# Kernel tuning notes

Hardware: AMD Instinct MI355X
Metric: run time of the kernel (lower is better)

## Reference

```python
import jax, jax.numpy as jnp
import numpy as np

B_SZ, T, D_IN, D_STATE, D_OUT = 32, 4096, 128, 128, 128


def setup_inputs() -> dict:
    key = jax.random.key(0)
    k1, k2, k3, k4, k5 = jax.random.split(key, 5)
    inputs = jax.random.normal(k1, (B_SZ, T, D_IN), dtype=jnp.float32)
    # A ~ orthogonal initializer scaled to spectral radius 0.9 for a stable recurrence
    Araw = jax.random.normal(k2, (D_STATE, D_STATE), dtype=jnp.float32)
    Q, _ = jnp.linalg.qr(Araw)
    A = 0.9 * Q
    B = jax.random.normal(k3, (D_STATE, D_IN), dtype=jnp.float32) / np.sqrt(D_IN)
    C = jax.random.normal(k4, (D_OUT, D_STATE), dtype=jnp.float32) / np.sqrt(D_STATE)
    D = jax.random.normal(k5, (D_OUT, D_IN), dtype=jnp.float32) / np.sqrt(D_IN)
    return {"inputs": inputs, "A": A, "B": B, "C": C, "D": D}


def reference(inputs, A, B, C, D):
    """x(t+1) = A x(t) + B u(t);  y(t+1) = C x(t+1) + D u(t).
    x0 = 0, return_sequences=True -> output [batch, time, d_out]."""
    x0 = jnp.zeros((inputs.shape[0], A.shape[0]), dtype=inputs.dtype)
    u_tb = jnp.swapaxes(inputs, 0, 1)  # [T, batch, d_in]

    def step(x, u):
        x1 = x @ A.T + u @ B.T          # [batch, d_state]
        y1 = x1 @ C.T + u @ D.T         # [batch, d_out]
        return x1, y1

    _, ys = jax.lax.scan(step, x0, u_tb)
    return jnp.swapaxes(ys, 0, 1)       # [batch, T, d_out]
```

## Files before the change

### kernel.cpp

```cpp
#include <hip/hip_runtime.h>
#include <cstddef>
#include <cstdint>

#define DIM 128
#define T_LEN 4096
#define BATCH 32
#define L_CH 32
#define N_CH 128
#define N_CHAINS 4096
#define KFULL 4096

typedef float f32x4 __attribute__((ext_vector_type(4)));
typedef short s16x8 __attribute__((ext_vector_type(8)));
typedef unsigned short u16x4 __attribute__((ext_vector_type(4)));
typedef unsigned short u16x8 __attribute__((ext_vector_type(8)));
typedef unsigned int u32;

#define OFF_UBF  0
#define OFF_A64  8388608
#define OFF_A96  8404992
#define OFF_A128 8421376
#define OFF_VBF  8437760
#define OFF_MCBF 8716288
#define OFF_VP2  8757248
#define OFF_SBF  12582912
#define OFF_KBF  12845056
#define OFF_CABF 13107200
#define OFF_WBF  13377536
#define OFF_AP   13639680
#define OFF_CA   14180352
#define OFF_K    14704640
#define OFF_W    15228928
#define OFF_B    15753216
#define OFF_C    15769600
#define OFF_D    15785984
#define AP(d)    (OFF_AP + (d) * 16384)

__device__ __forceinline__ f32x4 ld_pin(const float* p) {
    return *reinterpret_cast<const volatile f32x4*>(p);
}
__device__ __forceinline__ unsigned short f2bf(float x) {
    u32 u = __builtin_bit_cast(u32, x);
    return (unsigned short)((u + 0x7FFFu + ((u >> 16) & 1u)) >> 16);
}
__device__ __forceinline__ void gld16(const void* g, void* l) {
    __builtin_amdgcn_global_load_lds((const __attribute__((address_space(1))) u32*)g,
                                     (__attribute__((address_space(3))) u32*)l, 16, 0, 0);
}

__global__ void k_init(const float* __restrict__ u, const float* __restrict__ A,
                       const float* __restrict__ B, const float* __restrict__ C,
                       const float* __restrict__ D, float* __restrict__ wsf) {
    if (blockIdx.x < 8192) {
        unsigned short* ubf = (unsigned short*)(wsf + OFF_UBF);
        const size_t e0 = (size_t)(blockIdx.x * 256 + threadIdx.x) * 8;
        const f32x4 v0 = *reinterpret_cast<const f32x4*>(u + e0);
        const f32x4 v1 = *reinterpret_cast<const f32x4*>(u + e0 + 4);
        u16x8 o;
        o[0] = f2bf(v0.x); o[1] = f2bf(v0.y); o[2] = f2bf(v0.z); o[3] = f2bf(v0.w);
        o[4] = f2bf(v1.x); o[5] = f2bf(v1.y); o[6] = f2bf(v1.z); o[7] = f2bf(v1.w);
        *reinterpret_cast<u16x8*>(ubf + e0) = o;
    } else {
        const int e0 = ((blockIdx.x - 8192) * 256 + threadIdx.x) * 4;
        const int mat = e0 >> 14, rem = e0 & 16383;
        const float* src = (mat == 0) ? A : (mat == 1) ? B : (mat == 2) ? C : D;
        const int dst = (mat == 0) ? AP(1) : (mat == 1) ? OFF_B : (mat == 2) ? OFF_C : OFF_D;
        *reinterpret_cast<f32x4*>(wsf + dst + rem) =
            *reinterpret_cast<const f32x4*>(src + rem);
    }
}

__global__ void k_castm2(float* __restrict__ wsf) {
    const int e0 = (blockIdx.x * 256 + threadIdx.x) * 4;
    unsigned short* MCBF = (unsigned short*)(wsf + OFF_MCBF);
    unsigned short* WBF  = (unsigned short*)(wsf + OFF_WBF);
    u16x4 o;
    unsigned short* dst;
    if (e0 < 81920) {
        const int irow = e0 / 640;
        const int rem  = e0 - irow * 640;
        const int e    = rem >> 7;
        const int k    = rem & 127;
        if (e == 0) {
#pragma unroll
            for (int j = 0; j < 4; ++j)
                o[j] = (k + j == irow) ? (unsigned short)0x3F80 : (unsigned short)0;
        } else {
            const int moff = (e == 1) ? AP(32) : (e == 2) ? OFF_A64
                           : (e == 3) ? OFF_A96 : OFF_A128;
            const f32x4 v = *reinterpret_cast<const f32x4*>(wsf + moff + irow * 128 + k);
            o[0] = f2bf(v.x); o[1] = f2bf(v.y); o[2] = f2bf(v.z); o[3] = f2bf(v.w);
        }
        dst = MCBF + e0;
    } else {
        const int widx = e0 - 81920;
        const int i = widx >> 7, k = widx & 127;
        const f32x4 v = *reinterpret_cast<const f32x4*>(wsf + OFF_B + i * 128 + k);
        o[0] = f2bf(v.x); o[1] = f2bf(v.y); o[2] = f2bf(v.z); o[3] = f2bf(v.w);
        dst = WBF + i * 4096 + 3968 + k;
    }
    *reinterpret_cast<u16x4*>(dst) = o;
}

struct MMDesc { int n; int xo[64]; int yo[64]; int oo[64]; int ao[64]; int bo[64]; int bs[64]; };

__global__ __launch_bounds__(256, 1) void k_mmb(float* __restrict__ wsf, MMDesc d) {
    const int mm = blockIdx.x >> 2, sub = blockIdx.x & 3;
    const float* X = wsf + d.xo[mm];
    const float* Y = wsf + d.yo[mm];
    float* O = wsf + d.oo[mm];
    const int ao = d.ao[mm];
    __shared__ __align__(16) float Ys[DIM][DIM];
    const int t = threadIdx.x;
#pragma unroll
    for (int i = 0; i < 16; ++i) {
        const int j = t + i * 256;
        reinterpret_cast<f32x4*>(&Ys[0][0])[j] = reinterpret_cast<const f32x4*>(Y)[j];
    }
    const int r = sub * 32 + (t >> 3);
    const int c0 = (t & 7) * 16;
    f32x4 xr[32];
#pragma unroll
    for (int k = 0; k < 32; ++k) xr[k] = ld_pin(&X[r * DIM + 4 * k]);
    __syncthreads();
    float acc[16];
#pragma unroll
    for (int j = 0; j < 16; ++j) acc[j] = 0.f;
#pragma unroll
    for (int k = 0; k < DIM; ++k) {
        const float xv = ((const float*)xr)[k];
#pragma unroll
        for (int j = 0; j < 16; j += 4) {
            const f32x4 yv = *reinterpret_cast<const f32x4*>(&Ys[k][c0 + j]);
            acc[j + 0] = fmaf(xv, yv.x, acc[j + 0]);
            acc[j + 1] = fmaf(xv, yv.y, acc[j + 1]);
            acc[j + 2] = fmaf(xv, yv.z, acc[j + 2]);
            acc[j + 3] = fmaf(xv, yv.w, acc[j + 3]);
        }
    }
    if (ao >= 0) {
        const float* Ad = wsf + ao;
#pragma unroll
        for (int j = 0; j < 16; ++j) acc[j] += Ad[r * DIM + c0 + j];
    }
#pragma unroll
    for (int j = 0; j < 16; j += 4) {
        f32x4 o; o.x = acc[j]; o.y = acc[j + 1]; o.z = acc[j + 2]; o.w = acc[j + 3];
        *reinterpret_cast<f32x4*>(&O[r * DIM + c0 + j]) = o;
    }
    if (d.bo[mm] >= 0) {
        unsigned short* bw = (unsigned short*)wsf + (size_t)d.bo[mm] + (size_t)r * d.bs[mm] + c0;
#pragma unroll
        for (int j = 0; j < 16; j += 4) {
            u16x4 ob;
            ob[0] = f2bf(acc[j]); ob[1] = f2bf(acc[j + 1]);
            ob[2] = f2bf(acc[j + 2]); ob[3] = f2bf(acc[j + 3]);
            *reinterpret_cast<u16x4*>(bw + j) = ob;
        }
    }
}

__global__ __launch_bounds__(256, 2) void k_gemm1(const unsigned short* __restrict__ UBF,
                                                  const unsigned short* __restrict__ WBF,
                                                  float* __restrict__ VP) {
    __shared__ __align__(16) unsigned short lsA[2][4096];
    __shared__ __align__(16) unsigned short lsB[2][4096];
    const int b = blockIdx.x >> 2, ksp = blockIdx.x & 3;
    const int t = threadIdx.x, w = t >> 6, l = t & 63;
    const int wr = w >> 1, wc = w & 1;
    const int m0 = b * 128;
    const int rowA0 = w * 32 + (l >> 2);
    const int scol8 = ((l & 3) ^ ((l >> 3) & 3)) * 8;
    const int rsw   = ((l >> 4) ^ ((l >> 1) & 3)) * 8;
    const int wvb = w * 1024;
    const int kb = ksp * 1024;

    f32x4 acc[4][4];
#pragma unroll
    for (int a = 0; a < 4; ++a)
#pragma unroll
        for (int c = 0; c < 4; ++c) acc[a][c] = (f32x4)(0.f);

#define STAGE1(q, buf) do {                                                        \
    const int kq = kb + (q) * 32 + scol8;                                          \
    const unsigned short* ga = UBF + (size_t)(m0 + rowA0) * KFULL + kq;            \
    const unsigned short* gb = WBF + (size_t)rowA0 * KFULL + kq;                   \
    gld16(ga, &lsA[buf][wvb]);  gld16(ga + 16 * KFULL, &lsA[buf][wvb + 512]);      \
    gld16(gb, &lsB[buf][wvb]);  gld16(gb + 16 * KFULL, &lsB[buf][wvb + 512]);      \
} while (0)

    STAGE1(0, 0);
    __syncthreads();
#pragma unroll 1
    for (int q = 0; q < 32; ++q) {
        const int buf = q & 1;
        if (q + 1 < 32) STAGE1(q + 1, buf ^ 1);
        s16x8 af[4], bfr[4];
#pragma unroll
        for (int mi = 0; mi < 4; ++mi)
            af[mi] = *(const s16x8*)(&lsA[buf][(wr * 64 + mi * 16 + (l & 15)) * 32 + rsw]);
#pragma unroll
        for (int ni = 0; ni < 4; ++ni)
            bfr[ni] = *(const s16x8*)(&lsB[buf][(wc * 64 + ni * 16 + (l & 15)) * 32 + rsw]);
#pragma unroll
        for (int mi = 0; mi < 4; ++mi)
#pragma unroll
            for (int ni = 0; ni < 4; ++ni)
                acc[mi][ni] = __builtin_amdgcn_mfma_f32_16x16x32_bf16(af[mi], bfr[ni], acc[mi][ni], 0, 0, 0);
        __syncthreads();
    }
    float* vp = VP + (size_t)ksp * (N_CHAINS * DIM);
    const int row0 = wr * 64 + (l >> 4) * 4;
    const int col0 = wc * 64 + (l & 15);
#pragma unroll
    for (int mi = 0; mi < 4; ++mi)
#pragma unroll
        for (int ni = 0; ni < 4; ++ni)
#pragma unroll
            for (int jj = 0; jj < 4; ++jj)
                vp[(size_t)(m0 + row0 + mi * 16 + jj) * DIM + col0 + ni * 16] = acc[mi][ni][jj];
#undef STAGE1
}

__global__ void k_vred(const float* __restrict__ VP, unsigned short* __restrict__ VBF) {
    if (blockIdx.x < 512) {
        const int g = (blockIdx.x * 256 + threadIdx.x) * 4;
        f32x4 s = *reinterpret_cast<const f32x4*>(VP + g);
#pragma unroll
        for (int sp = 1; sp < 4; ++sp) {
            const f32x4 v = *reinterpret_cast<const f32x4*>(VP + sp * 524288 + g);
            s.x += v.x; s.y += v.y; s.z += v.z; s.w += v.w;
        }
        const int m = g >> 7, i = g & 127;
        const int b = m >> 7, c = m & 127;
        u16x4 o;
        o[0] = f2bf(s.x); o[1] = f2bf(s.y); o[2] = f2bf(s.z); o[3] = f2bf(s.w);
        *reinterpret_cast<u16x4*>(VBF + b * 17408 + (8 + c) * 128 + i) = o;
    } else {
        const int z = ((blockIdx.x - 512) * 256 + threadIdx.x) * 4;
        const int b = z >> 10, rem = z & 1023;
        u16x4 zz; zz[0] = 0; zz[1] = 0; zz[2] = 0; zz[3] = 0;
        *reinterpret_cast<u16x4*>(VBF + b * 17408 + rem) = zz;
    }
}

__global__ __launch_bounds__(256, 2) void k_comb2(const unsigned short* __restrict__ VBF,
                                                  const unsigned short* __restrict__ MCBF,
                                                  unsigned short* __restrict__ SBF) {
    __shared__ __align__(16) unsigned short lsA[2][4096];
    __shared__ __align__(16) unsigned short lsB[2][4096];
    const int b = blockIdx.x;
    const int t = threadIdx.x, w = t >> 6, l = t & 63;
    const int wr = w >> 1, wc = w & 1;
    const int rowA0 = w * 32 + (l >> 2);
    const int scol8 = ((l & 3) ^ ((l >> 3) & 3)) * 8;
    const int rsw   = ((l >> 4) ^ ((l >> 1) & 3)) * 8;
    const int wvb = w * 1024;
    const unsigned short* Vb = VBF + b * 17408;

    f32x4 acc[4][4];
#pragma unroll
    for (int a = 0; a < 4; ++a)
#pragma unroll
        for (int c = 0; c < 4; ++c) acc[a][c] = (f32x4)(0.f);

#define STAGEC(q, buf) do {                                                        \
    const int kq = (q) * 32 + scol8;                                               \
    const int e = kq >> 7, kk = kq & 127;                                          \
    const unsigned short* ga = Vb + (8 + rowA0 - 1 - e) * 128 + kk;                \
    const unsigned short* gb = MCBF + rowA0 * 640 + kq;                            \
    gld16(ga, &lsA[buf][wvb]);  gld16(ga + 16 * 128, &lsA[buf][wvb + 512]);        \
    gld16(gb, &lsB[buf][wvb]);  gld16(gb + 16 * 640, &lsB[buf][wvb + 512]);        \
} while (0)

    STAGEC(0, 0);
    __syncthreads();
#pragma unroll 1
    for (int q = 0; q < 20; ++q) {
        const int buf = q & 1;
        if (q + 1 < 20) STAGEC(q + 1, buf ^ 1);
        s16x8 af[4], bfr[4];
#pragma unroll
        for (int mi = 0; mi < 4; ++mi)
            af[mi] = *(const s16x8*)(&lsA[buf][(wr * 64 + mi * 16 + (l & 15)) * 32 + rsw]);
#pragma unroll
        for (int ni = 0; ni < 4; ++ni)
            bfr[ni] = *(const s16x8*)(&lsB[buf][(wc * 64 + ni * 16 + (l & 15)) * 32 + rsw]);
#pragma unroll
        for (int mi = 0; mi < 4; ++mi)
#pragma unroll
            for (int ni = 0; ni < 4; ++ni)
                acc[mi][ni] = __builtin_amdgcn_mfma_f32_16x16x32_bf16(af[mi], bfr[ni], acc[mi][ni], 0, 0, 0);
        __syncthreads();
    }
    const int row0 = wr * 64 + (l >> 4) * 4;
    const int col0 = wc * 64 + (l & 15);
#pragma unroll
    for (int mi = 0; mi < 4; ++mi)
#pragma unroll
        for (int ni = 0; ni < 4; ++ni)
#pragma unroll
            for (int jj = 0; jj < 4; ++jj)
                SBF[(size_t)(b * 128 + row0 + mi * 16 + jj) * 128 + col0 + ni * 16] =
                    f2bf(acc[mi][ni][jj]);
#undef STAGEC
}

__global__ __launch_bounds__(256, 2) void k_gemm3(const unsigned short* __restrict__ UBF,
                                                  const unsigned short* __restrict__ SBF,
                                                  const unsigned short* __restrict__ KBF,
                                                  const unsigned short* __restrict__ CABF,
                                                  float* __restrict__ out) {
    __shared__ __align__(16) unsigned short lsA[2][4096];
    __shared__ __align__(16) unsigned short lsB[2][4096];
    const int r = 31 - (blockIdx.x >> 5);
    const int bm = blockIdx.x & 31;
    const int t = threadIdx.x, w = t >> 6, l = t & 63;
    const int wr = w >> 1, wc = w & 1;
    const int m0 = bm * 128;
    const int rowA0 = w * 32 + (l >> 2);
    const int scol8 = ((l & 3) ^ ((l >> 3) & 3)) * 8;
    const int rsw   = ((l >> 4) ^ ((l >> 1) & 3)) * 8;
    const int wvb = w * 1024;
    const int NS = 4 * r + 8;

    f32x4 acc[4][4];
#pragma unroll
    for (int a = 0; a < 4; ++a)
#pragma unroll
        for (int c = 0; c < 4; ++c) acc[a][c] = (f32x4)(0.f);

#define STAGE3(q, buf) do {                                                            \
    const unsigned short *ga, *gb;  int strA, strB;                                    \
    if ((q) < 4 * (r + 1)) {                                                           \
        ga = UBF + (size_t)(m0 + rowA0) * KFULL + (q) * 32 + scol8;  strA = KFULL;     \
        gb = KBF + (size_t)(r - ((q) >> 2)) * 16384 + rowA0 * 128                      \
             + ((q) & 3) * 32 + scol8;                               strB = 128;       \
    } else {                                                                           \
        ga = SBF + (size_t)(m0 + rowA0) * 128 + ((q) & 3) * 32 + scol8;  strA = 128;   \
        gb = CABF + (size_t)(r + 1) * 16384 + rowA0 * 128 + ((q) & 3) * 32 + scol8;    \
        strB = 128;                                                                    \
    }                                                                                  \
    gld16(ga, &lsA[buf][wvb]);  gld16(ga + 16 * strA, &lsA[buf][wvb + 512]);           \
    gld16(gb, &lsB[buf][wvb]);  gld16(gb + 16 * strB, &lsB[buf][wvb + 512]);           \
} while (0)

    STAGE3(0, 0);
    __syncthreads();
#pragma unroll 1
    for (int q = 0; q < NS; ++q) {
        const int buf = q & 1;
        if (q + 1 < NS) STAGE3(q + 1, buf ^ 1);
        s16x8 af[4], bfr[4];
#pragma unroll
        for (int mi = 0; mi < 4; ++mi)
            af[mi] = *(const s16x8*)(&lsA[buf][(wr * 64 + mi * 16 + (l & 15)) * 32 + rsw]);
#pragma unroll
        for (int ni = 0; ni < 4; ++ni)
            bfr[ni] = *(const s16x8*)(&lsB[buf][(wc * 64 + ni * 16 + (l & 15)) * 32 + rsw]);
#pragma unroll
        for (int mi = 0; mi < 4; ++mi)
#pragma unroll
            for (int ni = 0; ni < 4; ++ni)
                acc[mi][ni] = __builtin_amdgcn_mfma_f32_16x16x32_bf16(af[mi], bfr[ni], acc[mi][ni], 0, 0, 0);
        __syncthreads();
    }
    const int row0 = wr * 64 + (l >> 4) * 4;
    const int col0 = wc * 64 + (l & 15);
#pragma unroll
    for (int mi = 0; mi < 4; ++mi)
#pragma unroll
        for (int ni = 0; ni < 4; ++ni)
#pragma unroll
            for (int jj = 0; jj < 4; ++jj)
                out[(size_t)(m0 + row0 + mi * 16 + jj) * KFULL + r * 128 + col0 + ni * 16] =
                    acc[mi][ni][jj];
#undef STAGE3
}

extern "C" void kernel_launch(void* const* d_in, const int* in_sizes, int n_in,
                              void* d_out, int out_size, void* d_ws, size_t ws_size,
                              hipStream_t stream) {
    const float* u  = (const float*)d_in[0];
    const float* Am = (const float*)d_in[1];
    const float* Bm = (const float*)d_in[2];
    const float* Cm = (const float*)d_in[3];
    const float* Dm = (const float*)d_in[4];
    float* out = (float*)d_out;
    float* wsf = (float*)d_ws;

    unsigned short* UBF  = (unsigned short*)(wsf + OFF_UBF);
    unsigned short* SBF  = (unsigned short*)(wsf + OFF_SBF);
    unsigned short* KBF  = (unsigned short*)(wsf + OFF_KBF);
    unsigned short* CABF = (unsigned short*)(wsf + OFF_CABF);
    unsigned short* WBF  = (unsigned short*)(wsf + OFF_WBF);
    unsigned short* VBF  = (unsigned short*)(wsf + OFF_VBF);
    unsigned short* MCBF = (unsigned short*)(wsf + OFF_MCBF);
    float* VP2 = wsf + OFF_VP2;

    const int KBF_U  = 2 * OFF_KBF;
    const int CABF_U = 2 * OFF_CABF;
    const int WBF_U  = 2 * OFF_WBF;

    hipLaunchKernelGGL(k_init, dim3(8256), dim3(256), 0, stream, u, Am, Bm, Cm, Dm, wsf);

    MMDesc s;
    for (int i = 0; i < 64; ++i) { s.bo[i] = -1; s.bs[i] = 0; }
    s.n = 1; s.xo[0] = AP(1); s.yo[0] = AP(1); s.oo[0] = AP(2); s.ao[0] = -1;
    hipLaunchKernelGGL(k_mmb, dim3(4), dim3(256), 0, stream, wsf, s);
    s.n = 2;
    s.xo[0] = AP(2); s.yo[0] = AP(1); s.oo[0] = AP(3); s.ao[0] = -1;
    s.xo[1] = AP(2); s.yo[1] = AP(2); s.oo[1] = AP(4); s.ao[1] = -1;
    hipLaunchKernelGGL(k_mmb, dim3(8), dim3(256), 0, stream, wsf, s);
    s.n = 4;
    for (int i = 0; i < 4; ++i) { s.xo[i] = AP(4); s.yo[i] = AP(1 + i); s.oo[i] = AP(5 + i); s.ao[i] = -1; }
    hipLaunchKernelGGL(k_mmb, dim3(16), dim3(256), 0, stream, wsf, s);
    s.n = 8;
    for (int i = 0; i < 8; ++i) { s.xo[i] = AP(8); s.yo[i] = AP(1 + i); s.oo[i] = AP(9 + i); s.ao[i] = -1; }
    hipLaunchKernelGGL(k_mmb, dim3(32), dim3(256), 0, stream, wsf, s);
    s.n = 16;
    for (int i = 0; i < 16; ++i) { s.xo[i] = AP(16); s.yo[i] = AP(1 + i); s.oo[i] = AP(17 + i); s.ao[i] = -1; }
    hipLaunchKernelGGL(k_mmb, dim3(64), dim3(256), 0, stream, wsf, s);
    s.n = 34;
    for (int i = 0; i < 32; ++i) {
        s.xo[i] = OFF_C; s.yo[i] = AP(1 + i); s.oo[i] = OFF_CA + i * 16384; s.ao[i] = -1;
        s.bo[i] = CABF_U + (i + 1) * 16384; s.bs[i] = 128;
    }
    s.xo[32] = OFF_C;  s.yo[32] = OFF_B;  s.oo[32] = OFF_K;   s.ao[32] = OFF_D;
    s.bo[32] = KBF_U;  s.bs[32] = 128;
    s.xo[33] = AP(32); s.yo[33] = AP(32); s.oo[33] = OFF_A64; s.ao[33] = -1; s.bo[33] = -1;
    hipLaunchKernelGGL(k_mmb, dim3(136), dim3(256), 0, stream, wsf, s);
    s.n = 64;
    for (int i = 0; i < 31; ++i) {
        s.xo[i] = OFF_CA + i * 16384; s.yo[i] = OFF_B; s.oo[i] = OFF_K + (i + 1) * 16384; s.ao[i] = -1;
        s.bo[i] = KBF_U + (i + 1) * 16384; s.bs[i] = 128;
    }
    for (int j = 0; j < 31; ++j) {
        s.xo[31 + j] = AP(31 - j); s.yo[31 + j] = OFF_B; s.oo[31 + j] = OFF_W + j * 16384; s.ao[31 + j] = -1;
        s.bo[31 + j] = WBF_U + j * 128; s.bs[31 + j] = 4096;
    }
    s.xo[62] = OFF_A64; s.yo[62] = AP(32);  s.oo[62] = OFF_A96;  s.ao[62] = -1; s.bo[62] = -1;
    s.xo[63] = OFF_A64; s.yo[63] = OFF_A64; s.oo[63] = OFF_A128; s.ao[63] = -1; s.bo[63] = -1;
    hipLaunchKernelGGL(k_mmb, dim3(256), dim3(256), 0, stream, wsf, s);

    hipLaunchKernelGGL(k_castm2, dim3(96), dim3(256), 0, stream, wsf);
    hipLaunchKernelGGL(k_gemm1, dim3(128), dim3(256), 0, stream, UBF, WBF, VP2);
    hipLaunchKernelGGL(k_vred, dim3(544), dim3(256), 0, stream, VP2, VBF);
    hipLaunchKernelGGL(k_comb2, dim3(BATCH), dim3(256), 0, stream, VBF, MCBF, SBF);
    hipLaunchKernelGGL(k_gemm3, dim3(1024), dim3(256), 0, stream, UBF, SBF, KBF, CABF, out);
}
```

Measured before the change: 341.2 us.

## Reschedule power-matrix launches, fuse partial reduction into combine, shorten combine depth

Reorganizes the precomputation schedule so the C·A^i, A^j·B and K products are built by doubling alongside the A powers across fewer, wider launches, dropping the final 64-matmul launch. It also folds the split-K partial-sum reduction and zero padding of VBF into the start of k_comb2, removing the separate k_vred launch. The combine step now uses powers up to A^64 only (3 blocks instead of 5), cutting its K-loop from 20 to 12 iterations and the MCBF cast work. The risk is that k_comb2 now runs the reduction on only 32 blocks, and the dependency chains in the rebuilt schedule must line up exactly.

```diff
diff --git a/kernel.cpp b/kernel.cpp
--- a/kernel.cpp
+++ b/kernel.cpp
@@ -18,8 +18,6 @@
 
 #define OFF_UBF  0
 #define OFF_A64  8388608
-#define OFF_A96  8404992
-#define OFF_A128 8421376
 #define OFF_VBF  8437760
 #define OFF_MCBF 8716288
 #define OFF_VP2  8757248
@@ -35,6 +33,10 @@
 #define OFF_C    15769600
 #define OFF_D    15785984
 #define AP(d)    (OFF_AP + (d) * 16384)
+
+#define KBF_U  (2 * OFF_KBF)
+#define CABF_U (2 * OFF_CABF)
+#define WBF_U  (2 * OFF_WBF)
 
 __device__ __forceinline__ f32x4 ld_pin(const float* p) {
     return *reinterpret_cast<const volatile f32x4*>(p);
@@ -76,9 +78,9 @@
     unsigned short* WBF  = (unsigned short*)(wsf + OFF_WBF);
     u16x4 o;
     unsigned short* dst;
-    if (e0 < 81920) {
-        const int irow = e0 / 640;
-        const int rem  = e0 - irow * 640;
+    if (e0 < 49152) {
+        const int irow = e0 / 384;
+        const int rem  = e0 - irow * 384;
         const int e    = rem >> 7;
         const int k    = rem & 127;
         if (e == 0) {
@@ -86,14 +88,13 @@
             for (int j = 0; j < 4; ++j)
                 o[j] = (k + j == irow) ? (unsigned short)0x3F80 : (unsigned short)0;
         } else {
-            const int moff = (e == 1) ? AP(32) : (e == 2) ? OFF_A64
-                           : (e == 3) ? OFF_A96 : OFF_A128;
+            const int moff = (e == 1) ? AP(32) : OFF_A64;
             const f32x4 v = *reinterpret_cast<const f32x4*>(wsf + moff + irow * 128 + k);
             o[0] = f2bf(v.x); o[1] = f2bf(v.y); o[2] = f2bf(v.z); o[3] = f2bf(v.w);
         }
         dst = MCBF + e0;
     } else {
-        const int widx = e0 - 81920;
+        const int widx = e0 - 49152;
         const int i = widx >> 7, k = widx & 127;
         const f32x4 v = *reinterpret_cast<const f32x4*>(wsf + OFF_B + i * 128 + k);
         o[0] = f2bf(v.x); o[1] = f2bf(v.y); o[2] = f2bf(v.z); o[3] = f2bf(v.w);
@@ -222,30 +223,9 @@
 #undef STAGE1
 }
 
-__global__ void k_vred(const float* __restrict__ VP, unsigned short* __restrict__ VBF) {
-    if (blockIdx.x < 512) {
-        const int g = (blockIdx.x * 256 + threadIdx.x) * 4;
-        f32x4 s = *reinterpret_cast<const f32x4*>(VP + g);
-#pragma unroll
-        for (int sp = 1; sp < 4; ++sp) {
-            const f32x4 v = *reinterpret_cast<const f32x4*>(VP + sp * 524288 + g);
-            s.x += v.x; s.y += v.y; s.z += v.z; s.w += v.w;
-        }
-        const int m = g >> 7, i = g & 127;
-        const int b = m >> 7, c = m & 127;
-        u16x4 o;
-        o[0] = f2bf(s.x); o[1] = f2bf(s.y); o[2] = f2bf(s.z); o[3] = f2bf(s.w);
-        *reinterpret_cast<u16x4*>(VBF + b * 17408 + (8 + c) * 128 + i) = o;
-    } else {
-        const int z = ((blockIdx.x - 512) * 256 + threadIdx.x) * 4;
-        const int b = z >> 10, rem = z & 1023;
-        u16x4 zz; zz[0] = 0; zz[1] = 0; zz[2] = 0; zz[3] = 0;
-        *reinterpret_cast<u16x4*>(VBF + b * 17408 + rem) = zz;
-    }
-}
-
-__global__ __launch_bounds__(256, 2) void k_comb2(const unsigned short* __restrict__ VBF,
+__global__ __launch_bounds__(256, 2) void k_comb2(const float* __restrict__ VP,
                                                   const unsigned short* __restrict__ MCBF,
+                                                  unsigned short* __restrict__ VBF,
                                                   unsigned short* __restrict__ SBF) {
     __shared__ __align__(16) unsigned short lsA[2][4096];
     __shared__ __align__(16) unsigned short lsB[2][4096];
@@ -256,7 +236,28 @@
     const int scol8 = ((l & 3) ^ ((l >> 3) & 3)) * 8;
     const int rsw   = ((l >> 4) ^ ((l >> 1) & 3)) * 8;
     const int wvb = w * 1024;
-    const unsigned short* Vb = VBF + b * 17408;
+    unsigned short* Vb = VBF + b * 17408;
+
+    {
+        u16x4 z; z[0] = 0; z[1] = 0; z[2] = 0; z[3] = 0;
+        *reinterpret_cast<u16x4*>(Vb + t * 4) = z;
+        const int base = b * 16384;
+#pragma unroll
+        for (int it = 0; it < 16; ++it) {
+            const int local = (it * 256 + t) * 4;
+            const int g = base + local;
+            f32x4 s = *reinterpret_cast<const f32x4*>(VP + g);
+#pragma unroll
+            for (int sp = 1; sp < 4; ++sp) {
+                const f32x4 v = *reinterpret_cast<const f32x4*>(VP + sp * 524288 + g);
+                s.x += v.x; s.y += v.y; s.z += v.z; s.w += v.w;
+            }
+            u16x4 o;
+            o[0] = f2bf(s.x); o[1] = f2bf(s.y); o[2] = f2bf(s.z); o[3] = f2bf(s.w);
+            *reinterpret_cast<u16x4*>(Vb + 1024 + local) = o;
+        }
+    }
+    __syncthreads();
 
     f32x4 acc[4][4];
 #pragma unroll
@@ -268,17 +269,17 @@
     const int kq = (q) * 32 + scol8;                                               \
     const int e = kq >> 7, kk = kq & 127;                                          \
     const unsigned short* ga = Vb + (8 + rowA0 - 1 - e) * 128 + kk;                \
-    const unsigned short* gb = MCBF + rowA0 * 640 + kq;                            \
+    const unsigned short* gb = MCBF + rowA0 * 384 + kq;                            \
     gld16(ga, &lsA[buf][wvb]);  gld16(ga + 16 * 128, &lsA[buf][wvb + 512]);        \
-    gld16(gb, &lsB[buf][wvb]);  gld16(gb + 16 * 640, &lsB[buf][wvb + 512]);        \
+    gld16(gb, &lsB[buf][wvb]);  gld16(gb + 16 * 384, &lsB[buf][wvb + 512]);        \
 } while (0)
 
     STAGEC(0, 0);
     __syncthreads();
 #pragma unroll 1
-    for (int q = 0; q < 20; ++q) {
+    for (int q = 0; q < 12; ++q) {
         const int buf = q & 1;
-        if (q + 1 < 20) STAGEC(q + 1, buf ^ 1);
+        if (q + 1 < 12) STAGEC(q + 1, buf ^ 1);
         s16x8 af[4], bfr[4];
 #pragma unroll
         for (int mi = 0; mi < 4; ++mi)
@@ -398,54 +399,88 @@
     unsigned short* MCBF = (unsigned short*)(wsf + OFF_MCBF);
     float* VP2 = wsf + OFF_VP2;
 
-    const int KBF_U  = 2 * OFF_KBF;
-    const int CABF_U = 2 * OFF_CABF;
-    const int WBF_U  = 2 * OFF_WBF;
-
     hipLaunchKernelGGL(k_init, dim3(8256), dim3(256), 0, stream, u, Am, Bm, Cm, Dm, wsf);
 
     MMDesc s;
-    for (int i = 0; i < 64; ++i) { s.bo[i] = -1; s.bs[i] = 0; }
-    s.n = 1; s.xo[0] = AP(1); s.yo[0] = AP(1); s.oo[0] = AP(2); s.ao[0] = -1;
-    hipLaunchKernelGGL(k_mmb, dim3(4), dim3(256), 0, stream, wsf, s);
-    s.n = 2;
-    s.xo[0] = AP(2); s.yo[0] = AP(1); s.oo[0] = AP(3); s.ao[0] = -1;
-    s.xo[1] = AP(2); s.yo[1] = AP(2); s.oo[1] = AP(4); s.ao[1] = -1;
-    hipLaunchKernelGGL(k_mmb, dim3(8), dim3(256), 0, stream, wsf, s);
-    s.n = 4;
-    for (int i = 0; i < 4; ++i) { s.xo[i] = AP(4); s.yo[i] = AP(1 + i); s.oo[i] = AP(5 + i); s.ao[i] = -1; }
-    hipLaunchKernelGGL(k_mmb, dim3(16), dim3(256), 0, stream, wsf, s);
-    s.n = 8;
-    for (int i = 0; i < 8; ++i) { s.xo[i] = AP(8); s.yo[i] = AP(1 + i); s.oo[i] = AP(9 + i); s.ao[i] = -1; }
-    hipLaunchKernelGGL(k_mmb, dim3(32), dim3(256), 0, stream, wsf, s);
-    s.n = 16;
-    for (int i = 0; i < 16; ++i) { s.xo[i] = AP(16); s.yo[i] = AP(1 + i); s.oo[i] = AP(17 + i); s.ao[i] = -1; }
-    hipLaunchKernelGGL(k_mmb, dim3(64), dim3(256), 0, stream, wsf, s);
-    s.n = 34;
+    auto reset = [&s]() { for (int i = 0; i < 64; ++i) { s.ao[i] = -1; s.bo[i] = -1; s.bs[i] = 0; } };
+
+    reset(); s.n = 3;
+    s.xo[0] = AP(1); s.yo[0] = AP(1); s.oo[0] = AP(2);
+    s.xo[1] = OFF_C; s.yo[1] = AP(1); s.oo[1] = OFF_CA;
+    s.bo[1] = CABF_U + 1 * 16384; s.bs[1] = 128;
+    s.xo[2] = AP(1); s.yo[2] = OFF_B; s.oo[2] = OFF_W + 16384;
+    s.bo[2] = WBF_U + 30 * 128; s.bs[2] = 4096;
+    hipLaunchKernelGGL(k_mmb, dim3(12), dim3(256), 0, stream, wsf, s);
+
+    reset(); s.n = 5;
+    s.xo[0] = AP(2); s.yo[0] = AP(1); s.oo[0] = AP(3);
+    s.xo[1] = AP(2); s.yo[1] = AP(2); s.oo[1] = AP(4);
+    s.xo[2] = OFF_CA; s.yo[2] = AP(1); s.oo[2] = OFF_CA + 16384;
+    s.bo[2] = CABF_U + 2 * 16384; s.bs[2] = 128;
+    s.xo[3] = AP(2); s.yo[3] = OFF_B; s.oo[3] = OFF_W + 2 * 16384;
+    s.bo[3] = WBF_U + 29 * 128; s.bs[3] = 4096;
+    s.xo[4] = AP(2); s.yo[4] = OFF_W + 16384; s.oo[4] = OFF_W + 3 * 16384;
+    s.bo[4] = WBF_U + 28 * 128; s.bs[4] = 4096;
+    hipLaunchKernelGGL(k_mmb, dim3(20), dim3(256), 0, stream, wsf, s);
+
+    reset(); s.n = 10;
+    for (int i = 0; i < 4; ++i) { s.xo[i] = AP(4); s.yo[i] = AP(1 + i); s.oo[i] = AP(5 + i); }
+    for (int j = 0; j < 2; ++j) {
+        s.xo[4 + j] = OFF_CA + j * 16384; s.yo[4 + j] = AP(2);
+        s.oo[4 + j] = OFF_CA + (2 + j) * 16384;
+        s.bo[4 + j] = CABF_U + (3 + j) * 16384; s.bs[4 + j] = 128;
+    }
+    for (int j = 0; j < 4; ++j) {
+        s.xo[6 + j] = AP(4); s.yo[6 + j] = (j == 0) ? OFF_B : OFF_W + j * 16384;
+        s.oo[6 + j] = OFF_W + (4 + j) * 16384;
+        s.bo[6 + j] = WBF_U + (31 - (4 + j)) * 128; s.bs[6 + j] = 4096;
+    }
+    hipLaunchKernelGGL(k_mmb, dim3(40), dim3(256), 0, stream, wsf, s);
+
+    reset(); s.n = 20;
+    for (int i = 0; i < 8; ++i) { s.xo[i] = AP(8); s.yo[i] = AP(1 + i); s.oo[i] = AP(9 + i); }
+    for (int j = 0; j < 4; ++j) {
+        s.xo[8 + j] = OFF_CA + j * 16384; s.yo[8 + j] = AP(4);
+        s.oo[8 + j] = OFF_CA + (4 + j) * 16384;
+        s.bo[8 + j] = CABF_U + (5 + j) * 16384; s.bs[8 + j] = 128;
+    }
+    for (int j = 0; j < 8; ++j) {
+        s.xo[12 + j] = AP(8); s.yo[12 + j] = (j == 0) ? OFF_B : OFF_W + j * 16384;
+        s.oo[12 + j] = OFF_W + (8 + j) * 16384;
+        s.bo[12 + j] = WBF_U + (31 - (8 + j)) * 128; s.bs[12 + j] = 4096;
+    }
+    hipLaunchKernelGGL(k_mmb, dim3(80), dim3(256), 0, stream, wsf, s);
+
+    reset(); s.n = 40;
+    for (int i = 0; i < 16; ++i) { s.xo[i] = AP(16); s.yo[i] = AP(1 + i); s.oo[i] = AP(17 + i); }
+    for (int j = 0; j < 8; ++j) {
+        s.xo[16 + j] = OFF_CA + j * 16384; s.yo[16 + j] = AP(8);
+        s.oo[16 + j] = OFF_CA + (8 + j) * 16384;
+        s.bo[16 + j] = CABF_U + (9 + j) * 16384; s.bs[16 + j] = 128;
+    }
+    for (int j = 0; j < 16; ++j) {
+        s.xo[24 + j] = AP(16); s.yo[24 + j] = (j == 0) ? OFF_B : OFF_W + j * 16384;
+        s.oo[24 + j] = OFF_W + (16 + j) * 16384;
+        s.bo[24 + j] = WBF_U + (31 - (16 + j)) * 128; s.bs[24 + j] = 4096;
+    }
+    hipLaunchKernelGGL(k_mmb, dim3(160), dim3(256), 0, stream, wsf, s);
+
+    reset(); s.n = 49;
     for (int i = 0; i < 32; ++i) {
-        s.xo[i] = OFF_C; s.yo[i] = AP(1 + i); s.oo[i] = OFF_CA + i * 16384; s.ao[i] = -1;
-        s.bo[i] = CABF_U + (i + 1) * 16384; s.bs[i] = 128;
-    }
-    s.xo[32] = OFF_C;  s.yo[32] = OFF_B;  s.oo[32] = OFF_K;   s.ao[32] = OFF_D;
-    s.bo[32] = KBF_U;  s.bs[32] = 128;
-    s.xo[33] = AP(32); s.yo[33] = AP(32); s.oo[33] = OFF_A64; s.ao[33] = -1; s.bo[33] = -1;
-    hipLaunchKernelGGL(k_mmb, dim3(136), dim3(256), 0, stream, wsf, s);
-    s.n = 64;
-    for (int i = 0; i < 31; ++i) {
-        s.xo[i] = OFF_CA + i * 16384; s.yo[i] = OFF_B; s.oo[i] = OFF_K + (i + 1) * 16384; s.ao[i] = -1;
-        s.bo[i] = KBF_U + (i + 1) * 16384; s.bs[i] = 128;
-    }
-    for (int j = 0; j < 31; ++j) {
-        s.xo[31 + j] = AP(31 - j); s.yo[31 + j] = OFF_B; s.oo[31 + j] = OFF_W + j * 16384; s.ao[31 + j] = -1;
-        s.bo[31 + j] = WBF_U + j * 128; s.bs[31 + j] = 4096;
-    }
-    s.xo[62] = OFF_A64; s.yo[62] = AP(32);  s.oo[62] = OFF_A96;  s.ao[62] = -1; s.bo[62] = -1;
-    s.xo[63] = OFF_A64; s.yo[63] = OFF_A64; s.oo[63] = OFF_A128; s.ao[63] = -1; s.bo[63] = -1;
-    hipLaunchKernelGGL(k_mmb, dim3(256), dim3(256), 0, stream, wsf, s);
-
-    hipLaunchKernelGGL(k_castm2, dim3(96), dim3(256), 0, stream, wsf);
+        s.xo[i] = OFF_C; s.yo[i] = (i == 0) ? OFF_B : OFF_W + i * 16384;
+        s.oo[i] = OFF_K + i * 16384; s.ao[i] = (i == 0) ? OFF_D : -1;
+        s.bo[i] = KBF_U + i * 16384; s.bs[i] = 128;
+    }
+    for (int j = 0; j < 16; ++j) {
+        s.xo[32 + j] = OFF_CA + j * 16384; s.yo[32 + j] = AP(16);
+        s.oo[32 + j] = OFF_CA + (16 + j) * 16384;
+        s.bo[32 + j] = CABF_U + (17 + j) * 16384; s.bs[32 + j] = 128;
+    }
+    s.xo[48] = AP(32); s.yo[48] = AP(32); s.oo[48] = OFF_A64;
+    hipLaunchKernelGGL(k_mmb, dim3(196), dim3(256), 0, stream, wsf, s);
+
+    hipLaunchKernelGGL(k_castm2, dim3(64), dim3(256), 0, stream, wsf);
     hipLaunchKernelGGL(k_gemm1, dim3(128), dim3(256), 0, stream, UBF, WBF, VP2);
-    hipLaunchKernelGGL(k_vred, dim3(544), dim3(256), 0, stream, VP2, VBF);
-    hipLaunchKernelGGL(k_comb2, dim3(BATCH), dim3(256), 0, stream, VBF, MCBF, SBF);
+    hipLaunchKernelGGL(k_comb2, dim3(BATCH), dim3(256), 0, stream, VP2, MCBF, VBF, SBF);
     hipLaunchKernelGGL(k_gemm3, dim3(1024), dim3(256), 0, stream, UBF, SBF, KBF, CABF, out);
 }
```

Measured after the change: 328.4 us. -3.8%, faster.
